# Optimization experiments

Hardware: AMD Instinct MI355X
Metric: run time of the kernel (lower is better)

## Reference

```python
import jax, jax.numpy as jnp
import numpy as np

B, S, H = 4, 2048, 1024

def setup_inputs() -> dict:
    key = jax.random.key(0)
    ks = jax.random.split(key, 4)
    scale = 1.0 / np.sqrt(H)
    x = jax.random.normal(ks[0], (B, S, H), dtype=jnp.float32)
    Wq = jax.random.normal(ks[1], (H, H), dtype=jnp.float32) * scale
    Wk = jax.random.normal(ks[2], (H, H), dtype=jnp.float32) * scale
    Wv = jax.random.normal(ks[3], (H, H), dtype=jnp.float32) * scale
    bq = jnp.zeros((H,), dtype=jnp.float32)
    bk = jnp.zeros((H,), dtype=jnp.float32)
    bv = jnp.zeros((H,), dtype=jnp.float32)
    return {"x": x, "Wq": Wq, "bq": bq, "Wk": Wk, "bk": bk, "Wv": Wv, "bv": bv}

def reference(x, Wq, bq, Wk, bk, Wv, bv):
    # Linear: y = x @ W^T + b (torch nn.Linear convention)
    Q = jnp.einsum('bsh,oh->bso', x, Wq) + bq
    K = jnp.einsum('bsh,oh->bso', x, Wk) + bk
    V = jnp.einsum('bsh,oh->bso', x, Wv) + bv
    scores = jnp.einsum('bqh,bkh->bqk', Q, K) / jnp.sqrt(jnp.float32(H))
    attn = jax.nn.softmax(scores, axis=-1)
    return jnp.einsum('bqk,bkh->bqh', attn, V)
```

## Files before the change

### kernel.cpp

```cpp
#include <hip/hip_runtime.h>
#include <cstdint>
#include <cstddef>


typedef __bf16 bf16;
typedef _Float16 f16;
typedef __bf16 bf16x8 __attribute__((ext_vector_type(8)));
typedef __bf16 bf16x4 __attribute__((ext_vector_type(4)));
typedef float f32x4 __attribute__((ext_vector_type(4)));

#define BM 128
#define BN 128
#define BK 64

#define XQ (8388608 / 4)
#define WQ (1048576 / 4)
__global__ __launch_bounds__(256)
void cvt_all(const float* __restrict__ x, const float* __restrict__ Wq,
             const float* __restrict__ Wk, const float* __restrict__ Wv,
             bf16* __restrict__ xb, bf16* __restrict__ Wqkv)
{
    const int i = blockIdx.x * 256 + threadIdx.x;
    const float* src;
    bf16* dst;
    if (i < XQ) {
        src = x + 4 * (size_t)i;
        dst = xb + 4 * (size_t)i;
    } else {
        const int j = i - XQ;
        const int w = j / WQ;
        const int off = j - w * WQ;
        const float* ws_ = (w == 0) ? Wq : (w == 1) ? Wk : Wv;
        src = ws_ + 4 * (size_t)off;
        dst = Wqkv + 4 * (size_t)j;
    }
    f32x4 v = *(const f32x4*)src;
    bf16x4 o;
#pragma unroll
    for (int r = 0; r < 4; ++r) o[r] = (bf16)v[r];
    *(bf16x4*)dst = o;
}

__device__ __forceinline__ void stage_tile(const bf16* __restrict__ g, int ld,
                                           bf16* lds_generic, int tid)
{
    auto lds3 = (__attribute__((address_space(3))) char*)lds_generic;
    const int wave = tid >> 6;
#pragma unroll
    for (int issue = 0; issue < 4; ++issue) {
        const int p   = issue * 256 + tid;
        const int row = p >> 3;
        const int cp  = p & 7;
        const int c   = cp ^ (row & 7);
        const bf16* gp = g + (size_t)row * ld + c * 8;
        const unsigned wave_base = (unsigned)(issue * 4096 + wave * 1024);
        __builtin_amdgcn_global_load_lds(
            (const __attribute__((address_space(1))) void*)gp,
            (__attribute__((address_space(3))) void*)(lds3 + wave_base),
            16, 0, 0);
    }
}

__device__ __forceinline__ bf16x8 read_frag(const bf16* lds, int row, int chunk)
{
    const int cp = chunk ^ (row & 7);
    return *(const bf16x8*)(lds + row * BK + cp * 8);
}

template <int OUTMODE, int DBUF>
__global__ __launch_bounds__(256, DBUF ? 2 : 4)
void gemm_bt(const bf16* __restrict__ A, const bf16* __restrict__ Bm,
             const float* __restrict__ bias0, const float* __restrict__ bias1,
             const float* __restrict__ bias2, void* __restrict__ C,
             int K, int N, float alpha, long zA, long zB, long zC)
{
    __shared__ alignas(16) bf16 As[DBUF + 1][BM * BK];
    __shared__ alignas(16) bf16 Bs[DBUF + 1][BN * BK];

    const int tid  = threadIdx.x;
    const int lane = tid & 63;
    const int wid  = tid >> 6;
    const int wr   = (wid >> 1) * 64;
    const int wc   = (wid & 1) * 64;
    const int quad = lane >> 4;
    const int l16  = lane & 15;

    const int m0 = blockIdx.y * BM;
    const int n0 = blockIdx.x * BN;
    const int z  = blockIdx.z;

    const bf16* Ab = A + (size_t)z * zA + (size_t)m0 * K;
    const bf16* Bb = Bm + (size_t)z * zB + (size_t)n0 * K;

    f32x4 acc[4][4] = {};

    if (DBUF) {
        stage_tile(Ab, K, As[0], tid);
        stage_tile(Bb, K, Bs[0], tid);
    }

    const int niter = K / BK;
    for (int it = 0; it < niter; ++it) {
        int cur;
        if (DBUF) {
            cur = it & 1;
            __syncthreads();
            if (it + 1 < niter) {
                stage_tile(Ab + (it + 1) * BK, K, As[cur ^ 1], tid);
                stage_tile(Bb + (it + 1) * BK, K, Bs[cur ^ 1], tid);
            }
        } else {
            cur = 0;
            __syncthreads();
            stage_tile(Ab + it * BK, K, As[0], tid);
            stage_tile(Bb + it * BK, K, Bs[0], tid);
            __syncthreads();
        }
#pragma unroll
        for (int h = 0; h < 2; ++h) {
            bf16x8 af[4], bfr[4];
#pragma unroll
            for (int i = 0; i < 4; ++i)
                af[i]  = read_frag(As[cur], wr + i * 16 + l16, h * 4 + quad);
#pragma unroll
            for (int j = 0; j < 4; ++j)
                bfr[j] = read_frag(Bs[cur], wc + j * 16 + l16, h * 4 + quad);

#pragma unroll
            for (int i = 0; i < 4; ++i)
#pragma unroll
                for (int j = 0; j < 4; ++j)
                    acc[i][j] = __builtin_amdgcn_mfma_f32_16x16x32_bf16(
                        af[i], bfr[j], acc[i][j], 0, 0, 0);
        }
    }

#pragma unroll
    for (int j = 0; j < 4; ++j) {
        const int col3 = n0 + wc + j * 16 + l16;
#pragma unroll
        for (int i = 0; i < 4; ++i) {
            const int rbase = m0 + wr + i * 16 + quad * 4;
            if (OUTMODE == 2) {
                f16* Cf = (f16*)C + (size_t)z * zC;
#pragma unroll
                for (int r = 0; r < 4; ++r)
                    Cf[(size_t)(rbase + r) * N + col3] = (f16)(acc[i][j][r] * alpha);
            } else if (OUTMODE == 3) {
                float* Cf = (float*)C + (size_t)z * zC;
#pragma unroll
                for (int r = 0; r < 4; ++r)
                    Cf[(size_t)(rbase + r) * N + col3] = acc[i][j][r];
            } else {
                const int mat = col3 >> 10;
                const int col = col3 & 1023;
                const float* bp = (mat == 0) ? bias0 : (mat == 1) ? bias1 : bias2;
                const float bj = bp[col];
                if (mat < 2) {
                    bf16* Cb = (bf16*)C + (size_t)mat * (8u << 20);
#pragma unroll
                    for (int r = 0; r < 4; ++r)
                        Cb[(size_t)(rbase + r) * 1024 + col] =
                            (bf16)(acc[i][j][r] + bj);
                } else {
                    bf16* Cb = (bf16*)C + (size_t)(16u << 20);
                    const int b = rbase >> 11;
                    const int s = rbase & 2047;
                    bf16x4 tmp;
#pragma unroll
                    for (int r = 0; r < 4; ++r) tmp[r] = (bf16)(acc[i][j][r] + bj);
                    *(bf16x4*)(Cb + (((size_t)((b << 10) + col)) << 11) + s) = tmp;
                }
            }
        }
    }
}

__device__ __forceinline__ float wred_max(float v)
{
#pragma unroll
    for (int o = 32; o > 0; o >>= 1) v = fmaxf(v, __shfl_xor(v, o, 64));
    return v;
}
__device__ __forceinline__ float wred_sum(float v)
{
#pragma unroll
    for (int o = 32; o > 0; o >>= 1) v += __shfl_xor(v, o, 64);
    return v;
}

__global__ __launch_bounds__(256)
void softmax_rows(const f16* __restrict__ Sc, bf16* __restrict__ P)
{
    constexpr int NC = 2048;
    const size_t row = blockIdx.x;
    const f16* src = Sc + row * NC;
    bf16* dst = P + row * NC;
    const int tid = threadIdx.x;

    float v[8];
    float m = -3.4e38f;
#pragma unroll
    for (int i = 0; i < 8; ++i) {
        v[i] = (float)src[tid + 256 * i];
        m = fmaxf(m, v[i]);
    }
    m = wred_max(m);

    __shared__ float redm[4], reds[4];
    if ((tid & 63) == 0) redm[tid >> 6] = m;
    __syncthreads();
    m = fmaxf(fmaxf(redm[0], redm[1]), fmaxf(redm[2], redm[3]));

    float s = 0.f;
#pragma unroll
    for (int i = 0; i < 8; ++i) { v[i] = __expf(v[i] - m); s += v[i]; }
    s = wred_sum(s);
    if ((tid & 63) == 0) reds[tid >> 6] = s;
    __syncthreads();
    s = reds[0] + reds[1] + reds[2] + reds[3];

    const float inv = 1.f / s;
#pragma unroll
    for (int i = 0; i < 8; ++i) dst[tid + 256 * i] = (bf16)(v[i] * inv);
}

extern "C" void kernel_launch(void* const* d_in, const int* in_sizes, int n_in,
                              void* d_out, int out_size, void* d_ws, size_t ws_size,
                              hipStream_t stream)
{
    constexpr int B = 4, S = 2048, H = 1024;
    const float* x  = (const float*)d_in[0];
    const float* Wq = (const float*)d_in[1];
    const float* bq = (const float*)d_in[2];
    const float* Wk = (const float*)d_in[3];
    const float* bk = (const float*)d_in[4];
    const float* Wv = (const float*)d_in[5];
    const float* bv = (const float*)d_in[6];
    float* out = (float*)d_out;

    char* ws = (char*)d_ws;
    bf16* xb   = (bf16*)ws;
    bf16* Wqkv = (bf16*)(ws + (size_t)(16 << 20));
    bf16* Q    = (bf16*)(ws + (size_t)(22 << 20));
    bf16* Kp   = (bf16*)(ws + (size_t)(38 << 20));
    bf16* Vt   = (bf16*)(ws + (size_t)(54 << 20));
    f16*  Sc   = (f16*) (ws + (size_t)(70 << 20));
    bf16* P    = (bf16*)(ws + (size_t)(22 << 20));

    dim3 blk(256, 1, 1);

    cvt_all<<<dim3((XQ + 3 * WQ) / 256), blk, 0, stream>>>(
        x, Wq, Wk, Wv, xb, Wqkv);

    gemm_bt<4, 1><<<dim3(3 * H / BN, (B * S) / BM, 1), blk, 0, stream>>>(
        xb, Wqkv, bq, bk, bv, Q, H, 3 * H, 1.0f, 0, 0, 0);

    gemm_bt<2, 0><<<dim3(S / BN, S / BM, B), blk, 0, stream>>>(
        Q, Kp, nullptr, nullptr, nullptr, Sc, H, S, 0.03125f,
        (long)S * H, (long)S * H, (long)S * S);

    softmax_rows<<<dim3(B * S), blk, 0, stream>>>(Sc, P);

    gemm_bt<3, 0><<<dim3(H / BN, S / BM, B), blk, 0, stream>>>(
        P, Vt, nullptr, nullptr, nullptr, out, S, H, 1.0f,
        (long)S * S, (long)H * S, (long)S * H);
}
```

Measured before the change: 261.5 us.

## Replace GEMMs with 256x256 tiles, 4-stage LDS pipeline and 8 waves

Replaces the 128x128 GEMM kernel with a 256x256-tile, 512-thread kernel. It uses a four-slot ring of 32-wide K tiles in 128 KB of dynamic LDS, three tiles prefetched ahead, and explicit vmcnt/barrier scheduling interleaved with MFMA bursts raised in priority. The larger tiles aim to cut global/LDS traffic per flop and hide load latency. The softmax also moves to vectorized 8-element loads and stores. Risks include fewer blocks on the smaller GEMMs (e.g. 128 blocks for the PV GEMM), higher register pressure from the 8x4 accumulators, and the hand-written wait counts depending on the exact load ordering.

Result: slower. 302.7 us (+15.7%).

```diff
diff --git a/kernel.cpp b/kernel.cpp
--- a/kernel.cpp
+++ b/kernel.cpp
@@ -7,11 +7,15 @@
 typedef _Float16 f16;
 typedef __bf16 bf16x8 __attribute__((ext_vector_type(8)));
 typedef __bf16 bf16x4 __attribute__((ext_vector_type(4)));
+typedef _Float16 f16x8 __attribute__((ext_vector_type(8)));
 typedef float f32x4 __attribute__((ext_vector_type(4)));
 
-#define BM 128
-#define BN 128
-#define BK 64
+#define BM 256
+#define BN 256
+#define BK 32
+#define UNIT_BYTES 16384
+#define BBASE 65536
+#define LDS_TOTAL 131072
 
 #define XQ (8388608 / 4)
 #define WQ (1048576 / 4)
@@ -41,49 +45,30 @@
     *(bf16x4*)dst = o;
 }
 
-__device__ __forceinline__ void stage_tile(const bf16* __restrict__ g, int ld,
-                                           bf16* lds_generic, int tid)
-{
-    auto lds3 = (__attribute__((address_space(3))) char*)lds_generic;
-    const int wave = tid >> 6;
-#pragma unroll
-    for (int issue = 0; issue < 4; ++issue) {
-        const int p   = issue * 256 + tid;
-        const int row = p >> 3;
-        const int cp  = p & 7;
-        const int c   = cp ^ (row & 7);
-        const bf16* gp = g + (size_t)row * ld + c * 8;
-        const unsigned wave_base = (unsigned)(issue * 4096 + wave * 1024);
-        __builtin_amdgcn_global_load_lds(
-            (const __attribute__((address_space(1))) void*)gp,
-            (__attribute__((address_space(3))) void*)(lds3 + wave_base),
-            16, 0, 0);
-    }
-}
-
-__device__ __forceinline__ bf16x8 read_frag(const bf16* lds, int row, int chunk)
-{
-    const int cp = chunk ^ (row & 7);
-    return *(const bf16x8*)(lds + row * BK + cp * 8);
-}
-
-template <int OUTMODE, int DBUF>
-__global__ __launch_bounds__(256, DBUF ? 2 : 4)
-void gemm_bt(const bf16* __restrict__ A, const bf16* __restrict__ Bm,
+__device__ __forceinline__ int frag_off(int row, int chunk)
+{
+    const int line = row >> 1;
+    const int pos = ((chunk << 1) | (row & 1)) ^ (line & 7);
+    return line * 128 + pos * 16;
+}
+
+template <int OUTMODE>
+__global__ __launch_bounds__(512, 2)
+void gemm256(const bf16* __restrict__ A, const bf16* __restrict__ Bm,
              const float* __restrict__ bias0, const float* __restrict__ bias1,
              const float* __restrict__ bias2, void* __restrict__ C,
              int K, int N, float alpha, long zA, long zB, long zC)
 {
-    __shared__ alignas(16) bf16 As[DBUF + 1][BM * BK];
-    __shared__ alignas(16) bf16 Bs[DBUF + 1][BN * BK];
+    extern __shared__ __align__(16) bf16 smem[];
+    auto lds3 = (__attribute__((address_space(3))) char*)smem;
 
     const int tid  = threadIdx.x;
     const int lane = tid & 63;
     const int wid  = tid >> 6;
-    const int wr   = (wid >> 1) * 64;
-    const int wc   = (wid & 1) * 64;
     const int quad = lane >> 4;
     const int l16  = lane & 15;
+    const int wr   = (wid >> 2) * 128;
+    const int wc   = (wid & 3) * 64;
 
     const int m0 = blockIdx.y * BM;
     const int n0 = blockIdx.x * BN;
@@ -92,54 +77,96 @@
     const bf16* Ab = A + (size_t)z * zA + (size_t)m0 * K;
     const bf16* Bb = Bm + (size_t)z * zB + (size_t)n0 * K;
 
-    f32x4 acc[4][4] = {};
-
-    if (DBUF) {
-        stage_tile(Ab, K, As[0], tid);
-        stage_tile(Bb, K, Bs[0], tid);
-    }
-
-    const int niter = K / BK;
-    for (int it = 0; it < niter; ++it) {
-        int cur;
-        if (DBUF) {
-            cur = it & 1;
-            __syncthreads();
-            if (it + 1 < niter) {
-                stage_tile(Ab + (it + 1) * BK, K, As[cur ^ 1], tid);
-                stage_tile(Bb + (it + 1) * BK, K, Bs[cur ^ 1], tid);
-            }
-        } else {
-            cur = 0;
-            __syncthreads();
-            stage_tile(Ab + it * BK, K, As[0], tid);
-            stage_tile(Bb + it * BK, K, Bs[0], tid);
-            __syncthreads();
-        }
-#pragma unroll
-        for (int h = 0; h < 2; ++h) {
-            bf16x8 af[4], bfr[4];
-#pragma unroll
-            for (int i = 0; i < 4; ++i)
-                af[i]  = read_frag(As[cur], wr + i * 16 + l16, h * 4 + quad);
+    int soff0, soff1;
+    {
+        const int s0 = tid, s1 = 512 + tid;
+        int line = s0 >> 3, un = (s0 & 7) ^ (line & 7);
+        soff0 = ((line << 1) | (un & 1)) * K + (un >> 1) * 8;
+        line = s1 >> 3; un = (s1 & 7) ^ (line & 7);
+        soff1 = ((line << 1) | (un & 1)) * K + (un >> 1) * 8;
+    }
+    const unsigned wb0 = (unsigned)(wid * 1024);
+
+#define STAGE(gsrc, ldsbase)                                                   \
+    do {                                                                       \
+        __builtin_amdgcn_global_load_lds(                                      \
+            (const __attribute__((address_space(1))) void*)((gsrc) + soff0),   \
+            (__attribute__((address_space(3))) void*)(lds3 + (ldsbase) + wb0), \
+            16, 0, 0);                                                         \
+        __builtin_amdgcn_global_load_lds(                                      \
+            (const __attribute__((address_space(1))) void*)((gsrc) + soff1),   \
+            (__attribute__((address_space(3))) void*)(lds3 + (ldsbase) + 8192 + wb0), \
+            16, 0, 0);                                                         \
+    } while (0)
+
+    int aoff[8], boff[4];
+#pragma unroll
+    for (int i = 0; i < 8; ++i) aoff[i] = frag_off(wr + i * 16 + l16, quad);
+#pragma unroll
+    for (int j = 0; j < 4; ++j) boff[j] = frag_off(wc + j * 16 + l16, quad);
+
+    const int NT = K / BK;
+    f32x4 acc[8][4] = {};
+
+#pragma unroll
+    for (int tt = 0; tt < 3; ++tt) {
+        STAGE(Ab + tt * BK, (unsigned)(tt * UNIT_BYTES));
+        STAGE(Bb + tt * BK, (unsigned)(BBASE + tt * UNIT_BYTES));
+    }
+    asm volatile("s_waitcnt vmcnt(8)\n\ts_barrier" ::: "memory");
+
+#pragma unroll 4
+    for (int t = 0; t < NT; ++t) {
+        const char* Au = (const char*)smem + (t & 3) * UNIT_BYTES;
+        const char* Bu = (const char*)smem + BBASE + (t & 3) * UNIT_BYTES;
+        bf16x8 af[4], bfr[4];
+
+#pragma unroll
+        for (int i = 0; i < 4; ++i) af[i] = *(const bf16x8*)(Au + aoff[i]);
+#pragma unroll
+        for (int j = 0; j < 4; ++j) bfr[j] = *(const bf16x8*)(Bu + boff[j]);
+        if (t < NT - 3)
+            STAGE(Ab + (t + 3) * BK, (unsigned)(((t + 3) & 3) * UNIT_BYTES));
+        asm volatile("s_barrier\n\ts_waitcnt lgkmcnt(0)" ::: "memory");
+        __builtin_amdgcn_s_setprio(1);
+#pragma unroll
+        for (int i = 0; i < 4; ++i)
 #pragma unroll
             for (int j = 0; j < 4; ++j)
-                bfr[j] = read_frag(Bs[cur], wc + j * 16 + l16, h * 4 + quad);
-
-#pragma unroll
-            for (int i = 0; i < 4; ++i)
-#pragma unroll
-                for (int j = 0; j < 4; ++j)
-                    acc[i][j] = __builtin_amdgcn_mfma_f32_16x16x32_bf16(
-                        af[i], bfr[j], acc[i][j], 0, 0, 0);
-        }
-    }
+                acc[i][j] = __builtin_amdgcn_mfma_f32_16x16x32_bf16(
+                    af[i], bfr[j], acc[i][j], 0, 0, 0);
+        __builtin_amdgcn_s_setprio(0);
+        asm volatile("s_barrier" ::: "memory");
+
+#pragma unroll
+        for (int i = 0; i < 4; ++i) af[i] = *(const bf16x8*)(Au + aoff[4 + i]);
+        if (t < NT - 3)
+            STAGE(Bb + (t + 3) * BK, (unsigned)(BBASE + ((t + 3) & 3) * UNIT_BYTES));
+        asm volatile("s_barrier\n\ts_waitcnt lgkmcnt(0)" ::: "memory");
+        __builtin_amdgcn_s_setprio(1);
+#pragma unroll
+        for (int i = 0; i < 4; ++i)
+#pragma unroll
+            for (int j = 0; j < 4; ++j)
+                acc[4 + i][j] = __builtin_amdgcn_mfma_f32_16x16x32_bf16(
+                    af[i], bfr[j], acc[4 + i][j], 0, 0, 0);
+        __builtin_amdgcn_s_setprio(0);
+        if (t < NT - 3)
+            asm volatile("s_waitcnt vmcnt(8)\n\ts_barrier" ::: "memory");
+        else if (t == NT - 3)
+            asm volatile("s_waitcnt vmcnt(4)\n\ts_barrier" ::: "memory");
+        else if (t == NT - 2)
+            asm volatile("s_waitcnt vmcnt(0)\n\ts_barrier" ::: "memory");
+        else
+            asm volatile("s_barrier" ::: "memory");
+    }
+#undef STAGE
 
 #pragma unroll
     for (int j = 0; j < 4; ++j) {
         const int col3 = n0 + wc + j * 16 + l16;
 #pragma unroll
-        for (int i = 0; i < 4; ++i) {
+        for (int i = 0; i < 8; ++i) {
             const int rbase = m0 + wr + i * 16 + quad * 4;
             if (OUTMODE == 2) {
                 f16* Cf = (f16*)C + (size_t)z * zC;
@@ -198,11 +225,12 @@
     bf16* dst = P + row * NC;
     const int tid = threadIdx.x;
 
+    f16x8 in = *(const f16x8*)(src + tid * 8);
     float v[8];
     float m = -3.4e38f;
 #pragma unroll
     for (int i = 0; i < 8; ++i) {
-        v[i] = (float)src[tid + 256 * i];
+        v[i] = (float)in[i];
         m = fmaxf(m, v[i]);
     }
     m = wred_max(m);
@@ -221,8 +249,10 @@
     s = reds[0] + reds[1] + reds[2] + reds[3];
 
     const float inv = 1.f / s;
-#pragma unroll
-    for (int i = 0; i < 8; ++i) dst[tid + 256 * i] = (bf16)(v[i] * inv);
+    bf16x8 o;
+#pragma unroll
+    for (int i = 0; i < 8; ++i) o[i] = (bf16)(v[i] * inv);
+    *(bf16x8*)(dst + tid * 8) = o;
 }
 
 extern "C" void kernel_launch(void* const* d_in, const int* in_sizes, int n_in,
@@ -248,21 +278,36 @@
     f16*  Sc   = (f16*) (ws + (size_t)(70 << 20));
     bf16* P    = (bf16*)(ws + (size_t)(22 << 20));
 
+    static bool attr_done = false;
+    if (!attr_done) {
+        attr_done = true;
+        (void)hipFuncSetAttribute(reinterpret_cast<const void*>(gemm256<4>),
+                                  hipFuncAttributeMaxDynamicSharedMemorySize,
+                                  LDS_TOTAL);
+        (void)hipFuncSetAttribute(reinterpret_cast<const void*>(gemm256<2>),
+                                  hipFuncAttributeMaxDynamicSharedMemorySize,
+                                  LDS_TOTAL);
+        (void)hipFuncSetAttribute(reinterpret_cast<const void*>(gemm256<3>),
+                                  hipFuncAttributeMaxDynamicSharedMemorySize,
+                                  LDS_TOTAL);
+    }
+
     dim3 blk(256, 1, 1);
+    dim3 blk512(512, 1, 1);
 
     cvt_all<<<dim3((XQ + 3 * WQ) / 256), blk, 0, stream>>>(
         x, Wq, Wk, Wv, xb, Wqkv);
 
-    gemm_bt<4, 1><<<dim3(3 * H / BN, (B * S) / BM, 1), blk, 0, stream>>>(
+    gemm256<4><<<dim3(3 * H / BN, (B * S) / BM, 1), blk512, LDS_TOTAL, stream>>>(
         xb, Wqkv, bq, bk, bv, Q, H, 3 * H, 1.0f, 0, 0, 0);
 
-    gemm_bt<2, 0><<<dim3(S / BN, S / BM, B), blk, 0, stream>>>(
+    gemm256<2><<<dim3(S / BN, S / BM, B), blk512, LDS_TOTAL, stream>>>(
         Q, Kp, nullptr, nullptr, nullptr, Sc, H, S, 0.03125f,
         (long)S * H, (long)S * H, (long)S * S);
 
     softmax_rows<<<dim3(B * S), blk, 0, stream>>>(Sc, P);
 
-    gemm_bt<3, 0><<<dim3(H / BN, S / BM, B), blk, 0, stream>>>(
+    gemm256<3><<<dim3(H / BN, S / BM, B), blk512, LDS_TOTAL, stream>>>(
         P, Vt, nullptr, nullptr, nullptr, out, S, H, 1.0f,
         (long)S * S, (long)H * S, (long)S * H);
 }
```
